# Kernel tuning notes

Hardware: AMD Instinct MI355X
Metric: run time of the kernel (lower is better)

Reference implementation:

```python
import jax, jax.numpy as jnp
import numpy as np

B, T, D = 4, 8192, 768
H = 12
HD = D // H
DFF = 4 * D
EPS_ATT = 1e-6
EPS_LN = 1e-5


def _layernorm(x, g, b):
    mu = jnp.mean(x, axis=-1, keepdims=True)
    var = jnp.mean(jnp.square(x - mu), axis=-1, keepdims=True)
    return (x - mu) * jax.lax.rsqrt(var + EPS_LN) * g + b


def setup_inputs() -> dict:
    key = jax.random.key(0)
    ks = jax.random.split(key, 12)
    s = 1.0 / np.sqrt(D)
    sf = 1.0 / np.sqrt(DFF)
    return {
        "x": jax.random.normal(ks[0], (B, T, D), jnp.float32),
        "Wq": jax.random.uniform(ks[1], (D, D), jnp.float32, -s, s),
        "Wk": jax.random.uniform(ks[2], (D, D), jnp.float32, -s, s),
        "Wv": jax.random.uniform(ks[3], (D, D), jnp.float32, -s, s),
        "Wo": jax.random.uniform(ks[4], (D, D), jnp.float32, -s, s),
        "bo": jax.random.uniform(ks[5], (D,), jnp.float32, -s, s),
        "ln1_g": jnp.ones((D,), jnp.float32),
        "ln1_b": jnp.zeros((D,), jnp.float32),
        "ln2_g": jnp.ones((D,), jnp.float32),
        "ln2_b": jnp.zeros((D,), jnp.float32),
        "W1": jax.random.uniform(ks[6], (D, DFF), jnp.float32, -s, s),
        "b1": jax.random.uniform(ks[7], (DFF,), jnp.float32, -s, s),
        "W2": jax.random.uniform(ks[8], (DFF, D), jnp.float32, -sf, sf),
        "b2": jax.random.uniform(ks[9], (D,), jnp.float32, -sf, sf),
    }


def reference(x, Wq, Wk, Wv, Wo, bo, ln1_g, ln1_b, ln2_g, ln2_b, W1, b1, W2, b2):
    h = x
    xn = _layernorm(x, ln1_g, ln1_b)
    # QKV projections -> [B, H, T, HD]
    def heads(w):
        return (xn @ w).reshape(B, T, H, HD).transpose(0, 2, 1, 3)
    Q = jax.nn.elu(heads(Wq)) + 1.0
    K = jax.nn.elu(heads(Wk)) + 1.0
    V = heads(Wv)
    # linear attention: KV outer-product sum and K_sum normalization
    KV = jnp.einsum('bhtd,bhte->bhde', K, V)      # [B,H,HD,HD]
    K_sum = K.sum(axis=2)                          # [B,H,HD]
    Z = jnp.einsum('bhtd,bhd->bht', Q, K_sum) + EPS_ATT
    ctx = jnp.einsum('bhtd,bhde->bhte', Q, KV) / Z[..., None]
    att = ctx.transpose(0, 2, 1, 3).reshape(B, T, D) @ Wo + bo
    x = att + h  # dropout is identity in eval
    h = x
    xn = _layernorm(x, ln2_g, ln2_b)
    ff = jax.nn.gelu(xn @ W1 + b1, approximate=False) @ W2 + b2
    return ff + h
```

## Files before the change

### kernel.cpp

```cpp
#include <hip/hip_runtime.h>
#include <math.h>


#define DEV __device__ __forceinline__

typedef __attribute__((ext_vector_type(8))) short s16x8;
typedef __attribute__((ext_vector_type(4))) float f32x4;

static constexpr int    Bb   = 4;
static constexpr int    Tt   = 8192;
static constexpr int    Dd   = 768;
static constexpr int    Hh   = 12;
static constexpr size_t Mrows = (size_t)Bb * Tt;

DEV float bf2f(unsigned short u) {
    union { unsigned int i; float f; } c; c.i = ((unsigned int)u) << 16; return c.f;
}
DEV unsigned short f2bf(float f) {
    union { float f; unsigned int i; } c; c.f = f;
    unsigned int r = c.i + 0x7fffu + ((c.i >> 16) & 1u);
    return (unsigned short)(r >> 16);
}

DEV void gload16(const unsigned short* g, void* l) {
    __builtin_amdgcn_global_load_lds(
        (const __attribute__((address_space(1))) void*)g,
        (__attribute__((address_space(3))) void*)l, 16, 0, 0);
}

__global__ __launch_bounds__(256)
void transpose_f2b(const float* __restrict__ in, unsigned short* __restrict__ out,
                   int R, int C) {
    __shared__ float tile[32][33];
    const int c0 = blockIdx.x * 32, r0 = blockIdx.y * 32;
    const int tx = threadIdx.x, ty = threadIdx.y;
    #pragma unroll
    for (int i = 0; i < 32; i += 8)
        tile[ty + i][tx] = in[(size_t)(r0 + ty + i) * C + c0 + tx];
    __syncthreads();
    #pragma unroll
    for (int i = 0; i < 32; i += 8)
        out[(size_t)(c0 + ty + i) * R + r0 + tx] = f2bf(tile[tx][ty + i]);
}

template <int BF16IN>
__global__ __launch_bounds__(256)
void ln_kernel(const void* __restrict__ xin, const float* __restrict__ g,
               const float* __restrict__ bvec, unsigned short* __restrict__ out) {
    __shared__ float red[4];
    const int tid = threadIdx.x;
    const size_t base = (size_t)blockIdx.x * Dd;
    float v[3];
    #pragma unroll
    for (int i = 0; i < 3; ++i) {
        const size_t idx = base + tid + i * 256;
        if (BF16IN) v[i] = bf2f(((const unsigned short*)xin)[idx]);
        else        v[i] = ((const float*)xin)[idx];
    }
    float s = v[0] + v[1] + v[2];
    #pragma unroll
    for (int o = 32; o >= 1; o >>= 1) s += __shfl_xor(s, o);
    if ((tid & 63) == 0) red[tid >> 6] = s;
    __syncthreads();
    s = red[0] + red[1] + red[2] + red[3];
    const float mu = s * (1.0f / Dd);
    __syncthreads();
    float q = 0.f;
    #pragma unroll
    for (int i = 0; i < 3; ++i) { const float d = v[i] - mu; q += d * d; }
    #pragma unroll
    for (int o = 32; o >= 1; o >>= 1) q += __shfl_xor(q, o);
    if ((tid & 63) == 0) red[tid >> 6] = q;
    __syncthreads();
    q = red[0] + red[1] + red[2] + red[3];
    const float rstd = rsqrtf(q * (1.0f / Dd) + 1e-5f);
    #pragma unroll
    for (int i = 0; i < 3; ++i) {
        const int c = tid + i * 256;
        out[base + c] = f2bf((v[i] - mu) * rstd * g[c] + bvec[c]);
    }
}

#define EPI_QKV  0
#define EPI_X2   1
#define EPI_GELU 2
#define EPI_OUT1 3
#define EPI_OUT2 4

template <int EPI, int K, int PB, int BM>
__global__ __launch_bounds__(512, 2)
void gemm8p(const unsigned short* __restrict__ A,
            const unsigned short* __restrict__ BT,
            const float* __restrict__ bias,
            const void* __restrict__ res,
            void* __restrict__ out, int N) {
    constexpr int NT   = K / 64;
    constexpr int MF   = BM / 32;
    constexpr int RPW  = (BM + 256) / 64;
    constexpr int RBA  = BM / 8;
    constexpr int LDSB = (BM + 256) * 128;
    const int NTile = N >> 8;
    const int nwg = gridDim.x;
    int wg = blockIdx.x;
    wg = (wg & 7) * (nwg >> 3) + (wg >> 3);
    const int nt = wg % NTile, mt = wg / NTile;
    const int m0 = mt * BM, n0 = nt * 256;
    const int tid = threadIdx.x;
    const int lane = tid & 63, w = tid >> 6;
    const int wm = w >> 2, wn = w & 3;
    const int l15 = lane & 15, lk = lane >> 4;

    __shared__ __align__(16) char lds[2 * LDSB];

    const unsigned short* BTb = PB ? (BT + (size_t)(m0 >> 13) * 768 * 768) : BT;

    const int lr = lane >> 3;
    const int lg = (lane & 7) ^ lr;

    auto stage = [&](int t) {
        const size_t kcol = (size_t)(t << 6) + lg * 8;
        char* base = lds + (t & 1) * LDSB;
        #pragma unroll
        for (int j = 0; j < RPW; ++j) {
            const int rb = w * RPW + j;
            const unsigned short* src = (rb < RBA)
                ? A   + (size_t)(m0 + rb * 8 + lr) * K + kcol
                : BTb + (size_t)(n0 + (rb - RBA) * 8 + lr) * K + kcol;
            gload16(src, base + rb * 1024);
        }
    };

    f32x4 acc[MF][4] = {};

    auto ktile = [&](int d) {
        const char* bA = lds + d * LDSB + (wm * (BM / 2)) * 128;
        const char* bB = lds + d * LDSB + BM * 128 + (wn * 64) * 128;
        s16x8 bfr[4][2], afr[MF][2];
        #pragma unroll
        for (int nf = 0; nf < 4; ++nf)
            #pragma unroll
            for (int kk = 0; kk < 2; ++kk)
                bfr[nf][kk] = *(const s16x8*)(bB + (nf * 16 + l15) * 128 +
                                (((kk * 4 + lk) ^ (l15 & 7)) << 4));
        #pragma unroll
        for (int mf = 0; mf < MF; ++mf)
            #pragma unroll
            for (int kk = 0; kk < 2; ++kk)
                afr[mf][kk] = *(const s16x8*)(bA + (mf * 16 + l15) * 128 +
                                (((kk * 4 + lk) ^ (l15 & 7)) << 4));
        __builtin_amdgcn_s_setprio(1);
        #pragma unroll
        for (int mf = 0; mf < MF; ++mf)
            #pragma unroll
            for (int nf = 0; nf < 4; ++nf)
                #pragma unroll
                for (int kk = 0; kk < 2; ++kk)
                    acc[mf][nf] = __builtin_amdgcn_mfma_f32_16x16x32_bf16(
                        afr[mf][kk], bfr[nf][kk], acc[mf][nf], 0, 0, 0);
        __builtin_amdgcn_s_setprio(0);
    };

    stage(0);
    stage(1);
    for (int t = 0; t < NT; ++t) {
        if (t == NT - 1) asm volatile("s_waitcnt vmcnt(0)" ::: "memory");
        else             asm volatile("s_waitcnt vmcnt(%0)" :: "i"(RPW) : "memory");
        __builtin_amdgcn_s_barrier();
        ktile(t & 1);
        __builtin_amdgcn_s_barrier();
        if (t + 2 < NT) stage(t + 2);
    }

    #pragma unroll
    for (int mi = 0; mi < MF; ++mi) {
        #pragma unroll
        for (int nj = 0; nj < 4; ++nj) {
            const int col = n0 + wn * 64 + nj * 16 + l15;
            #pragma unroll
            for (int r = 0; r < 4; ++r) {
                const int row = m0 + wm * (BM / 2) + mi * 16 + lk * 4 + r;
                float v = acc[mi][nj][r];
                if (EPI == EPI_QKV) {
                    const int which = col / 768;
                    const int cc = col - which * 768;
                    if (which < 2) v = (v > 0.f) ? (v + 1.f) : __expf(v);
                    ((unsigned short*)out)[(size_t)which * (Mrows * Dd) + (size_t)row * Dd + cc] = f2bf(v);
                } else if (EPI == EPI_X2) {
                    v += bias[col] + ((const float*)res)[(size_t)row * N + col];
                    ((unsigned short*)out)[(size_t)row * N + col] = f2bf(v);
                } else if (EPI == EPI_GELU) {
                    v += bias[col];
                    v = 0.5f * v * (1.0f + erff(v * 0.70710678118654752f));
                    ((unsigned short*)out)[(size_t)row * N + col] = f2bf(v);
                } else if (EPI == EPI_OUT1) {
                    v += bias[col] + bf2f(((const unsigned short*)res)[(size_t)row * N + col]);
                    ((float*)out)[(size_t)row * N + col] = v;
                } else {
                    ((float*)out)[(size_t)row * N + col] += v;
                }
            }
        }
    }
}

__global__ __launch_bounds__(256)
void kv_partial(const unsigned short* __restrict__ Km, const unsigned short* __restrict__ Vm,
                float* __restrict__ part, float* __restrict__ pksum) {
    const int ck = blockIdx.x, bh = blockIdx.y;
    const int b = bh / Hh, h = bh - b * Hh;
    const int tid = threadIdx.x;
    const int e = tid & 63, dg = tid >> 6;
    __shared__ float sK[32][64], sV[32][64];
    float acc[16] = {};
    float ksacc = 0.f;
    const size_t rowbase = ((size_t)b * Tt + (size_t)ck * 1024) * Dd + h * 64;
    const int rw = tid >> 3, cv = (tid & 7) * 8;
    for (int ts = 0; ts < 1024; ts += 32) {
        const s16x8 k8 = *(const s16x8*)(Km + rowbase + (size_t)(ts + rw) * Dd + cv);
        const s16x8 v8 = *(const s16x8*)(Vm + rowbase + (size_t)(ts + rw) * Dd + cv);
        float kf[8], vf[8];
        #pragma unroll
        for (int j = 0; j < 8; ++j) {
            kf[j] = bf2f((unsigned short)k8[j]);
            vf[j] = bf2f((unsigned short)v8[j]);
        }
        __syncthreads();
        *(float4*)(&sK[rw][cv])     = *(const float4*)&kf[0];
        *(float4*)(&sK[rw][cv + 4]) = *(const float4*)&kf[4];
        *(float4*)(&sV[rw][cv])     = *(const float4*)&vf[0];
        *(float4*)(&sV[rw][cv + 4]) = *(const float4*)&vf[4];
        __syncthreads();
        #pragma unroll 4
        for (int tt = 0; tt < 32; ++tt) {
            const float vv = sV[tt][e];
            const float4* kp = (const float4*)(&sK[tt][dg * 16]);
            const float4 k0 = kp[0], k1 = kp[1], k2 = kp[2], k3 = kp[3];
            acc[0]  += k0.x * vv; acc[1]  += k0.y * vv; acc[2]  += k0.z * vv; acc[3]  += k0.w * vv;
            acc[4]  += k1.x * vv; acc[5]  += k1.y * vv; acc[6]  += k1.z * vv; acc[7]  += k1.w * vv;
            acc[8]  += k2.x * vv; acc[9]  += k2.y * vv; acc[10] += k2.z * vv; acc[11] += k2.w * vv;
            acc[12] += k3.x * vv; acc[13] += k3.y * vv; acc[14] += k3.z * vv; acc[15] += k3.w * vv;
        }
        if (dg == 0) {
            #pragma unroll 4
            for (int tt = 0; tt < 32; ++tt) ksacc += sK[tt][e];
        }
    }
    float* op = part + ((size_t)bh * 8 + ck) * 4096 + (size_t)dg * 16 * 64 + e;
    #pragma unroll
    for (int i = 0; i < 16; ++i) op[(size_t)i * 64] = acc[i];
    if (dg == 0) pksum[((size_t)bh * 8 + ck) * 64 + e] = ksacc;
}

__global__ __launch_bounds__(256)
void kv_reduce(const float* __restrict__ part, const float* __restrict__ pksum,
               float* __restrict__ kv, float* __restrict__ ksum) {
    const int bh = blockIdx.x;
    const int tid = threadIdx.x;
    #pragma unroll
    for (int j = 0; j < 16; ++j) {
        const int i = j * 256 + tid;
        float s = 0.f;
        #pragma unroll
        for (int c = 0; c < 8; ++c) s += part[((size_t)bh * 8 + c) * 4096 + i];
        kv[(size_t)bh * 4096 + i] = s;
    }
    if (tid < 64) {
        float s = 0.f;
        #pragma unroll
        for (int c = 0; c < 8; ++c) s += pksum[((size_t)bh * 8 + c) * 64 + tid];
        ksum[(size_t)bh * 64 + tid] = s;
    }
}

__global__ __launch_bounds__(256)
void qscale_kernel(unsigned short* __restrict__ Q, const float* __restrict__ ksum) {
    const int row = blockIdx.x;
    const int b = row >> 13;
    const int tid = threadIdx.x, lane = tid & 63;
    const size_t base = (size_t)row * Dd;
    #pragma unroll
    for (int i = 0; i < 3; ++i) {
        const int c = i * 256 + tid;
        const int h = c >> 6;
        const float q = bf2f(Q[base + c]);
        float zp = q * ksum[((size_t)b * Hh + h) * 64 + lane];
        #pragma unroll
        for (int o = 32; o >= 1; o >>= 1) zp += __shfl_xor(zp, o);
        const float zi = 1.0f / (zp + 1e-6f);
        Q[base + c] = f2bf(q * zi);
    }
}

__global__ __launch_bounds__(256)
void w2_build(const float* __restrict__ kvf, const unsigned short* __restrict__ woT,
              unsigned short* __restrict__ W2T) {
    const int bh = blockIdx.x, ny = blockIdx.y;
    const int b = bh / Hh, h = bh - b * Hh;
    __shared__ float sKV[64][65];
    const int tid = threadIdx.x;
    for (int i = tid; i < 4096; i += 256) sKV[i >> 6][i & 63] = kvf[(size_t)bh * 4096 + i];
    __syncthreads();
    const int d = tid & 63, ng = tid >> 6;
    #pragma unroll 4
    for (int i = 0; i < 48; ++i) {
        const int n = ny * 192 + i * 4 + ng;
        const unsigned short* wr = woT + (size_t)n * Dd + h * 64;
        float a = 0.f;
        #pragma unroll
        for (int e = 0; e < 64; ++e) a += bf2f(wr[e]) * sKV[d][e];
        W2T[((size_t)b * Dd + n) * Dd + h * 64 + d] = f2bf(a);
    }
}

extern "C" void kernel_launch(void* const* d_in, const int* in_sizes, int n_in,
                              void* d_out, int out_size, void* d_ws, size_t ws_size,
                              hipStream_t stream) {
    (void)in_sizes; (void)n_in; (void)out_size; (void)ws_size;
    const float* x    = (const float*)d_in[0];
    const float* Wq   = (const float*)d_in[1];
    const float* Wk   = (const float*)d_in[2];
    const float* Wv   = (const float*)d_in[3];
    const float* Wo   = (const float*)d_in[4];
    const float* bo   = (const float*)d_in[5];
    const float* ln1g = (const float*)d_in[6];
    const float* ln1b = (const float*)d_in[7];
    const float* ln2g = (const float*)d_in[8];
    const float* ln2b = (const float*)d_in[9];
    const float* W1   = (const float*)d_in[10];
    const float* b1   = (const float*)d_in[11];
    const float* W2   = (const float*)d_in[12];
    const float* b2   = (const float*)d_in[13];
    float* outp = (float*)d_out;

    char* ws = (char*)d_ws;
    const size_t SZ = Mrows * Dd * 2;
    unsigned short* xn = (unsigned short*)(ws + 0);
    unsigned short* Qb = (unsigned short*)(ws + SZ);
    unsigned short* Kb = (unsigned short*)(ws + 2 * SZ);
    unsigned short* Vb = (unsigned short*)(ws + 3 * SZ);
    char* p = ws + 4 * SZ;
    float* part  = (float*)p;  p += (size_t)48 * 8 * 4096 * 4;
    float* kvf   = (float*)p;  p += (size_t)48 * 4096 * 4;
    float* ksumf = (float*)p;  p += (size_t)48 * 64 * 4;
    unsigned short* wqkvT = (unsigned short*)p; p += (size_t)2304 * 768 * 2;
    unsigned short* woT   = (unsigned short*)p; p += (size_t)768 * 768 * 2;
    unsigned short* w1T   = (unsigned short*)p; p += (size_t)3072 * 768 * 2;
    unsigned short* w2aT  = (unsigned short*)p; p += (size_t)768 * 1536 * 2;
    unsigned short* w2bT  = (unsigned short*)p; p += (size_t)768 * 1536 * 2;
    float* pksum = (float*)p;  p += (size_t)48 * 8 * 64 * 4;
    unsigned short* W2T = (unsigned short*)part;
    unsigned short* ff1 = Qb;
    unsigned short* x2b = Vb;

    const dim3 blk(256);
    const dim3 tb(32, 8);

    transpose_f2b<<<dim3(24, 24), tb, 0, stream>>>(Wq, wqkvT, 768, 768);
    transpose_f2b<<<dim3(24, 24), tb, 0, stream>>>(Wk, wqkvT + 589824, 768, 768);
    transpose_f2b<<<dim3(24, 24), tb, 0, stream>>>(Wv, wqkvT + 2 * 589824, 768, 768);
    transpose_f2b<<<dim3(24, 24), tb, 0, stream>>>(Wo, woT, 768, 768);
    transpose_f2b<<<dim3(96, 24), tb, 0, stream>>>(W1, w1T, 768, 3072);
    transpose_f2b<<<dim3(24, 48), tb, 0, stream>>>(W2, w2aT, 1536, 768);
    transpose_f2b<<<dim3(24, 48), tb, 0, stream>>>(W2 + (size_t)1536 * 768, w2bT, 1536, 768);

    ln_kernel<0><<<32768, blk, 0, stream>>>(x, ln1g, ln1b, xn);

    gemm8p<EPI_QKV, 768, 0, 256><<<1152, 512, 0, stream>>>(xn, wqkvT, nullptr, nullptr, Qb, 2304);

    kv_partial<<<dim3(8, 48), blk, 0, stream>>>(Kb, Vb, part, pksum);
    kv_reduce<<<48, blk, 0, stream>>>(part, pksum, kvf, ksumf);

    qscale_kernel<<<32768, blk, 0, stream>>>(Qb, ksumf);
    w2_build<<<dim3(48, 4), blk, 0, stream>>>(kvf, woT, W2T);

    gemm8p<EPI_X2, 768, 1, 128><<<768, 512, 0, stream>>>(Qb, W2T, bo, x, x2b, 768);

    ln_kernel<1><<<32768, blk, 0, stream>>>(x2b, ln2g, ln2b, xn);

    gemm8p<EPI_GELU, 768, 0, 256><<<768, 512, 0, stream>>>(xn, w1T, b1, nullptr, ff1, 1536);
    gemm8p<EPI_OUT1, 1536, 0, 128><<<768, 512, 0, stream>>>(ff1, w2aT, b2, x2b, outp, 768);
    gemm8p<EPI_GELU, 768, 0, 256><<<768, 512, 0, stream>>>(xn, w1T + (size_t)1536 * 768,
                                                           b1 + 1536, nullptr, ff1, 1536);
    gemm8p<EPI_OUT2, 1536, 0, 128><<<768, 512, 0, stream>>>(ff1, w2bT, nullptr, nullptr, outp, 768);
}
```

Baseline: 1.091 ms.

## Restructure GEMM main loop into 4-stage K=32 pipeline with split compute phases

The GEMM kernel now uses K-tiles of 32 instead of 64, with a four-buffer LDS ring and three tiles prefetched ahead. Each iteration is split into two halves. Global loads for tile t+3 are issued between LDS fragment reads and MFMA bursts, and barriers are placed so loads overlap compute more finely. The QKV GEMM also moves from BM=256 to BM=128, doubling its grid size. The cost is more barriers per unit of work and a new swizzle pattern that has to stay bank-conflict free.

```diff
diff --git a/kernel.cpp b/kernel.cpp
--- a/kernel.cpp
+++ b/kernel.cpp
@@ -89,16 +89,16 @@
 
 template <int EPI, int K, int PB, int BM>
 __global__ __launch_bounds__(512, 2)
-void gemm8p(const unsigned short* __restrict__ A,
+void gemmfp(const unsigned short* __restrict__ A,
             const unsigned short* __restrict__ BT,
             const float* __restrict__ bias,
             const void* __restrict__ res,
             void* __restrict__ out, int N) {
-    constexpr int NT   = K / 64;
+    constexpr int NT   = K / 32;
     constexpr int MF   = BM / 32;
-    constexpr int RPW  = (BM + 256) / 64;
-    constexpr int RBA  = BM / 8;
-    constexpr int LDSB = (BM + 256) * 128;
+    constexpr int RPW  = (BM + 256) / 128;
+    constexpr int GA   = BM / 16;
+    constexpr int LDSB = (BM + 256) * 64;
     const int NTile = N >> 8;
     const int nwg = gridDim.x;
     int wg = blockIdx.x;
@@ -110,65 +110,72 @@
     const int wm = w >> 2, wn = w & 3;
     const int l15 = lane & 15, lk = lane >> 4;
 
-    __shared__ __align__(16) char lds[2 * LDSB];
+    __shared__ __align__(16) char lds[4 * LDSB];
 
     const unsigned short* BTb = PB ? (BT + (size_t)(m0 >> 13) * 768 * 768) : BT;
 
-    const int lr = lane >> 3;
-    const int lg = (lane & 7) ^ lr;
-
-    auto stage = [&](int t) {
-        const size_t kcol = (size_t)(t << 6) + lg * 8;
-        char* base = lds + (t & 1) * LDSB;
-        #pragma unroll
-        for (int j = 0; j < RPW; ++j) {
-            const int rb = w * RPW + j;
-            const unsigned short* src = (rb < RBA)
-                ? A   + (size_t)(m0 + rb * 8 + lr) * K + kcol
-                : BTb + (size_t)(n0 + (rb - RBA) * 8 + lr) * K + kcol;
-            gload16(src, base + rb * 1024);
+    const int srow = lane >> 2;
+    const int gsrc = (lane & 3) ^ ((lane >> 3) & 3);
+
+    auto stage = [&](int t, int j0, int j1) {
+        const size_t kcol = (size_t)(t << 5) + gsrc * 8;
+        char* base = lds + (t & 3) * LDSB;
+        #pragma unroll
+        for (int j = j0; j < j1; ++j) {
+            const int grp = w * RPW + j;
+            const unsigned short* src = (grp < GA)
+                ? A   + (size_t)(m0 + grp * 16 + srow) * K + kcol
+                : BTb + (size_t)(n0 + (grp - GA) * 16 + srow) * K + kcol;
+            gload16(src, base + grp * 1024);
         }
     };
 
     f32x4 acc[MF][4] = {};
-
-    auto ktile = [&](int d) {
-        const char* bA = lds + d * LDSB + (wm * (BM / 2)) * 128;
-        const char* bB = lds + d * LDSB + BM * 128 + (wn * 64) * 128;
-        s16x8 bfr[4][2], afr[MF][2];
-        #pragma unroll
-        for (int nf = 0; nf < 4; ++nf)
-            #pragma unroll
-            for (int kk = 0; kk < 2; ++kk)
-                bfr[nf][kk] = *(const s16x8*)(bB + (nf * 16 + l15) * 128 +
-                                (((kk * 4 + lk) ^ (l15 & 7)) << 4));
-        #pragma unroll
-        for (int mf = 0; mf < MF; ++mf)
-            #pragma unroll
-            for (int kk = 0; kk < 2; ++kk)
-                afr[mf][kk] = *(const s16x8*)(bA + (mf * 16 + l15) * 128 +
-                                (((kk * 4 + lk) ^ (l15 & 7)) << 4));
+    const int swb = ((l15 >> 1) & 3) << 4;
+
+    stage(0, 0, RPW); stage(1, 0, RPW); stage(2, 0, RPW);
+    asm volatile("s_waitcnt vmcnt(%0)" :: "i"(2 * RPW) : "memory");
+    __builtin_amdgcn_s_barrier();
+
+    for (int t = 0; t < NT; ++t) {
+        const char* bA = lds + (t & 3) * LDSB + (wm * (BM / 2)) * 64;
+        const char* bB = lds + (t & 3) * LDSB + BM * 64 + (wn * 64) * 64;
+        s16x8 af[MF], bf0, bf1;
+        #pragma unroll
+        for (int mf = 0; mf < MF; ++mf)
+            af[mf] = *(const s16x8*)(bA + (mf * 16 + l15) * 64 + ((lk << 4) ^ swb));
+        bf0 = *(const s16x8*)(bB + (l15) * 64 + ((lk << 4) ^ swb));
+        bf1 = *(const s16x8*)(bB + (16 + l15) * 64 + ((lk << 4) ^ swb));
+        if (t + 3 < NT) stage(t + 3, 0, 2);
+        __builtin_amdgcn_s_barrier();
+        asm volatile("s_waitcnt lgkmcnt(0)" ::: "memory");
         __builtin_amdgcn_s_setprio(1);
         #pragma unroll
         for (int mf = 0; mf < MF; ++mf)
-            #pragma unroll
-            for (int nf = 0; nf < 4; ++nf)
-                #pragma unroll
-                for (int kk = 0; kk < 2; ++kk)
-                    acc[mf][nf] = __builtin_amdgcn_mfma_f32_16x16x32_bf16(
-                        afr[mf][kk], bfr[nf][kk], acc[mf][nf], 0, 0, 0);
+            acc[mf][0] = __builtin_amdgcn_mfma_f32_16x16x32_bf16(af[mf], bf0, acc[mf][0], 0, 0, 0);
+        #pragma unroll
+        for (int mf = 0; mf < MF; ++mf)
+            acc[mf][1] = __builtin_amdgcn_mfma_f32_16x16x32_bf16(af[mf], bf1, acc[mf][1], 0, 0, 0);
         __builtin_amdgcn_s_setprio(0);
-    };
-
-    stage(0);
-    stage(1);
-    for (int t = 0; t < NT; ++t) {
-        if (t == NT - 1) asm volatile("s_waitcnt vmcnt(0)" ::: "memory");
-        else             asm volatile("s_waitcnt vmcnt(%0)" :: "i"(RPW) : "memory");
         __builtin_amdgcn_s_barrier();
-        ktile(t & 1);
+        s16x8 bf2, bf3;
+        bf2 = *(const s16x8*)(bB + (32 + l15) * 64 + ((lk << 4) ^ swb));
+        bf3 = *(const s16x8*)(bB + (48 + l15) * 64 + ((lk << 4) ^ swb));
+        if (t + 3 < NT) stage(t + 3, 2, RPW);
+        if (t < NT - 3)       asm volatile("s_waitcnt vmcnt(%0)" :: "i"(2 * RPW) : "memory");
+        else if (t == NT - 3) asm volatile("s_waitcnt vmcnt(%0)" :: "i"(RPW) : "memory");
+        else if (t == NT - 2) asm volatile("s_waitcnt vmcnt(0)" ::: "memory");
         __builtin_amdgcn_s_barrier();
-        if (t + 2 < NT) stage(t + 2);
+        asm volatile("s_waitcnt lgkmcnt(0)" ::: "memory");
+        __builtin_amdgcn_s_setprio(1);
+        #pragma unroll
+        for (int mf = 0; mf < MF; ++mf)
+            acc[mf][2] = __builtin_amdgcn_mfma_f32_16x16x32_bf16(af[mf], bf2, acc[mf][2], 0, 0, 0);
+        #pragma unroll
+        for (int mf = 0; mf < MF; ++mf)
+            acc[mf][3] = __builtin_amdgcn_mfma_f32_16x16x32_bf16(af[mf], bf3, acc[mf][3], 0, 0, 0);
+        __builtin_amdgcn_s_setprio(0);
+        __builtin_amdgcn_s_barrier();
     }
 
     #pragma unroll
@@ -365,7 +372,7 @@
 
     ln_kernel<0><<<32768, blk, 0, stream>>>(x, ln1g, ln1b, xn);
 
-    gemm8p<EPI_QKV, 768, 0, 256><<<1152, 512, 0, stream>>>(xn, wqkvT, nullptr, nullptr, Qb, 2304);
+    gemmfp<EPI_QKV, 768, 0, 128><<<2304, 512, 0, stream>>>(xn, wqkvT, nullptr, nullptr, Qb, 2304);
 
     kv_partial<<<dim3(8, 48), blk, 0, stream>>>(Kb, Vb, part, pksum);
     kv_reduce<<<48, blk, 0, stream>>>(part, pksum, kvf, ksumf);
@@ -373,13 +380,13 @@
     qscale_kernel<<<32768, blk, 0, stream>>>(Qb, ksumf);
     w2_build<<<dim3(48, 4), blk, 0, stream>>>(kvf, woT, W2T);
 
-    gemm8p<EPI_X2, 768, 1, 128><<<768, 512, 0, stream>>>(Qb, W2T, bo, x, x2b, 768);
+    gemmfp<EPI_X2, 768, 1, 128><<<768, 512, 0, stream>>>(Qb, W2T, bo, x, x2b, 768);
 
     ln_kernel<1><<<32768, blk, 0, stream>>>(x2b, ln2g, ln2b, xn);
 
-    gemm8p<EPI_GELU, 768, 0, 256><<<768, 512, 0, stream>>>(xn, w1T, b1, nullptr, ff1, 1536);
-    gemm8p<EPI_OUT1, 1536, 0, 128><<<768, 512, 0, stream>>>(ff1, w2aT, b2, x2b, outp, 768);
-    gemm8p<EPI_GELU, 768, 0, 256><<<768, 512, 0, stream>>>(xn, w1T + (size_t)1536 * 768,
+    gemmfp<EPI_GELU, 768, 0, 256><<<768, 512, 0, stream>>>(xn, w1T, b1, nullptr, ff1, 1536);
+    gemmfp<EPI_OUT1, 1536, 0, 128><<<768, 512, 0, stream>>>(ff1, w2aT, b2, x2b, outp, 768);
+    gemmfp<EPI_GELU, 768, 0, 256><<<768, 512, 0, stream>>>(xn, w1T + (size_t)1536 * 768,
                                                            b1 + 1536, nullptr, ff1, 1536);
-    gemm8p<EPI_OUT2, 1536, 0, 128><<<768, 512, 0, stream>>>(ff1, w2bT, nullptr, nullptr, outp, 768);
-}
+    gemmfp<EPI_OUT2, 1536, 0, 128><<<768, 512, 0, stream>>>(ff1, w2bT, nullptr, nullptr, outp, 768);
+}
```

Result: faster. 1.060 ms (-2.9%).
